# Kernel tuning notes

Hardware: AMD Instinct MI355X
Metric: run time of the kernel (lower is better)

The kernel has to match this reference:

```python
import jax, jax.numpy as jnp
import numpy as np

H = 1024
N_HEADS = 8
HEAD_DIM = H // N_HEADS
META_DIM = 256
VOCAB = 32000
MIN_W, MAX_W = 0.1, 5.0
LN_EPS = 1e-5


def _ln(x, g, b):
    mu = jnp.mean(x, axis=-1, keepdims=True)
    var = jnp.var(x, axis=-1, keepdims=True)
    return (x - mu) * jax.lax.rsqrt(var + LN_EPS) * g + b


def setup_inputs() -> dict:
    key = jax.random.key(0)
    ks = jax.random.split(key, 16)
    B, S = 4, 2048
    s = 0.02
    return {
        "hidden_states": jax.random.normal(ks[0], (B, S, H), jnp.float32),
        "token_ids": jax.random.randint(ks[1], (B, S), 0, VOCAB, jnp.int32),
        "attention_mask": jnp.ones((B, S), jnp.bool_),
        "pos_embed": jax.random.normal(ks[2], (1, S, H), jnp.float32),
        # torch nn.MultiheadAttention params
        "in_proj_w": jax.random.normal(ks[3], (3 * H, H), jnp.float32) * s,
        "in_proj_b": jnp.zeros((3 * H,), jnp.float32),
        "out_w": jax.random.normal(ks[4], (H, H), jnp.float32) * s,
        "out_b": jnp.zeros((H,), jnp.float32),
        # meta_network params (torch Linear convention: y = x @ W.T + b)
        "w1": jax.random.normal(ks[5], (META_DIM, 2 * H), jnp.float32) * s,
        "b1": jnp.zeros((META_DIM,), jnp.float32),
        "g1": jnp.ones((META_DIM,), jnp.float32),
        "beta1": jnp.zeros((META_DIM,), jnp.float32),
        "w2": jax.random.normal(ks[6], (META_DIM // 2, META_DIM), jnp.float32) * s,
        "b2": jnp.zeros((META_DIM // 2,), jnp.float32),
        "g2": jnp.ones((META_DIM // 2,), jnp.float32),
        "beta2": jnp.zeros((META_DIM // 2,), jnp.float32),
        "w3": jax.random.normal(ks[7], (1, META_DIM // 2), jnp.float32) * s,
        "b3": jnp.zeros((1,), jnp.float32),
        # tensorized ImportanceMemory.get_importance: one scalar per vocab id
        "importance_table": jax.random.uniform(ks[8], (VOCAB,), jnp.float32) * 0.1,
    }


def reference(hidden_states, token_ids, attention_mask, pos_embed,
              in_proj_w, in_proj_b, out_w, out_b,
              w1, b1, g1, beta1, w2, b2, g2, beta2, w3, b3,
              importance_table):
    B, S, _ = hidden_states.shape
    x = hidden_states + pos_embed[:, :S, :]

    # MultiheadAttention (batch_first, eval mode -> no dropout)
    qkv = x @ in_proj_w.T + in_proj_b                      # [B,S,3H]
    q, k, v = jnp.split(qkv, 3, axis=-1)
    q = q.reshape(B, S, N_HEADS, HEAD_DIM)
    k = k.reshape(B, S, N_HEADS, HEAD_DIM)
    v = v.reshape(B, S, N_HEADS, HEAD_DIM)
    scores = jnp.einsum('bqhd,bkhd->bhqk', q, k) / jnp.sqrt(jnp.float32(HEAD_DIM))
    scores = jnp.where(attention_mask[:, None, None, :], scores, jnp.float32(-1e9))
    attn = jax.nn.softmax(scores, axis=-1)
    ctx = jnp.einsum('bhqk,bkhd->bqhd', attn, v).reshape(B, S, H)
    attended = ctx @ out_w.T + out_b

    combined = jnp.concatenate([x, attended], axis=-1)     # [B,S,2H]
    h = jax.nn.relu(_ln(combined @ w1.T + b1, g1, beta1))
    h = jax.nn.relu(_ln(h @ w2.T + b2, g2, beta2))
    base_weights = (h @ w3.T + b3).squeeze(-1)             # [B,S]

    # tensorized per-token importance lookup + clamp (manual_weights empty)
    importance = importance_table[token_ids]               # gather [B,S]
    weight = jnp.clip(base_weights * (1.0 + importance), MIN_W, MAX_W)
    return jnp.where(attention_mask, weight, 0.0)
```

## Files before the change

kernel.cpp:

```cpp
#include <hip/hip_runtime.h>
#include <hip/hip_bf16.h>
#include <math.h>

typedef __bf16 bf16;
typedef bf16 bf16x8 __attribute__((ext_vector_type(8)));
typedef bf16 bf16x4 __attribute__((ext_vector_type(4)));
typedef float f32x4 __attribute__((ext_vector_type(4)));

#define HDIM 1024
#define NHEADS 8
#define HD 128
#define MD1 256
#define MD2 128
#define LNEPS 1e-5f

__device__ __forceinline__ f32x4 mfma16(bf16x8 a, bf16x8 b, f32x4 c) {
  return __builtin_amdgcn_mfma_f32_16x16x32_bf16(a, b, c, 0, 0, 0);
}

__device__ __forceinline__ void gload_lds16(const bf16* g, bf16* l) {
  __builtin_amdgcn_global_load_lds(
      (const __attribute__((address_space(1))) void*)g,
      (__attribute__((address_space(3))) void*)l, 16, 0, 0);
}

__global__ void k_prep_all(
    const float* __restrict__ hs, const float* __restrict__ pos,
    bf16* __restrict__ xbf, int SH, int nprep,
    const float* __restrict__ s0, bf16* __restrict__ d0, int n0,
    const float* __restrict__ s1, bf16* __restrict__ d1, int n1,
    const float* __restrict__ s2, bf16* __restrict__ d2, int n2,
    const float* __restrict__ s3, bf16* __restrict__ d3, int n3) {
  int i = (blockIdx.x * blockDim.x + threadIdx.x) * 4;
  if (i < nprep) {
    float4 a = *(const float4*)(hs + i);
    float4 p = *(const float4*)(pos + (i % SH));
    bf16x4 o;
    o[0] = (bf16)(a.x + p.x); o[1] = (bf16)(a.y + p.y);
    o[2] = (bf16)(a.z + p.z); o[3] = (bf16)(a.w + p.w);
    *(bf16x4*)(xbf + i) = o;
    return;
  }
  int j = i - nprep;
  const float* s; bf16* d;
  if (j < n0)                { s = s0 + j; d = d0 + j; }
  else if (j < n0 + n1)      { s = s1 + (j - n0); d = d1 + (j - n0); }
  else if (j < n0 + n1 + n2) { s = s2 + (j - n0 - n1); d = d2 + (j - n0 - n1); }
  else                       { s = s3 + (j - n0 - n1 - n2); d = d3 + (j - n0 - n1 - n2); }
  float4 v = *(const float4*)s;
  bf16x4 o;
  o[0] = (bf16)v.x; o[1] = (bf16)v.y; o[2] = (bf16)v.z; o[3] = (bf16)v.w;
  *(bf16x4*)d = o;
}

template<bool OUT_BF>
__global__ __launch_bounds__(256) void k_gemm128(
    const bf16* __restrict__ A, const bf16* __restrict__ Bw,
    const float* __restrict__ bias, void* __restrict__ out,
    int N, int K) {
  __shared__ bf16 As[128 * 32];
  __shared__ bf16 Bs[128 * 32];
  const int tid = threadIdx.x;
  const int w = tid >> 6, lane = tid & 63;
  const int quad = lane >> 4, l16 = lane & 15;
  const int wm = w & 1, wn = w >> 1;
  const int tm = blockIdx.x * 128, tn = blockIdx.y * 128;

  const int r0 = tid >> 2;
  const int f0 = (r0 ^ (r0 >> 2)) & 3;
  const int f1 = ((r0 + 64) ^ ((r0 + 64) >> 2)) & 3;
  const int c0 = (((tid & 3) ^ f0) * 8);
  const int c1 = (((tid & 3) ^ f1) * 8);
  const bf16* a0 = A + (size_t)(tm + r0) * K + c0;
  const bf16* a1 = A + (size_t)(tm + r0 + 64) * K + c1;
  const bf16* b0 = Bw + (size_t)(tn + r0) * K + c0;
  const bf16* b1 = Bw + (size_t)(tn + r0 + 64) * K + c1;
  bf16* lA = As + (size_t)tid * 8;
  bf16* lB = Bs + (size_t)tid * 8;

  f32x4 acc[4][4] = {};
  for (int k0 = 0; k0 < K; k0 += 32) {
    gload_lds16(a0 + k0, lA);
    gload_lds16(a1 + k0, lA + 2048);
    gload_lds16(b0 + k0, lB);
    gload_lds16(b1 + k0, lB + 2048);
    __syncthreads();
    bf16x8 af[4], bfr[4];
#pragma unroll
    for (int mt = 0; mt < 4; ++mt) {
      const int r = wm * 64 + mt * 16 + l16;
      af[mt] = *(const bf16x8*)&As[r * 32 + ((quad ^ ((r ^ (r >> 2)) & 3)) << 3)];
    }
#pragma unroll
    for (int nt = 0; nt < 4; ++nt) {
      const int r = wn * 64 + nt * 16 + l16;
      bfr[nt] = *(const bf16x8*)&Bs[r * 32 + ((quad ^ ((r ^ (r >> 2)) & 3)) << 3)];
    }
#pragma unroll
    for (int mt = 0; mt < 4; ++mt)
#pragma unroll
      for (int nt = 0; nt < 4; ++nt)
        acc[mt][nt] = mfma16(af[mt], bfr[nt], acc[mt][nt]);
    __syncthreads();
  }

#pragma unroll
  for (int nt = 0; nt < 4; ++nt) {
    const int col = tn + wn * 64 + nt * 16 + l16;
    const float bv = bias ? bias[col] : 0.f;
#pragma unroll
    for (int mt = 0; mt < 4; ++mt) {
#pragma unroll
      for (int i = 0; i < 4; ++i) {
        const int row = tm + wm * 64 + mt * 16 + quad * 4 + i;
        const float v = acc[mt][nt][i] + bv;
        if (OUT_BF) ((bf16*)out)[(size_t)row * N + col] = (bf16)v;
        else        ((float*)out)[(size_t)row * N + col] = v;
      }
    }
  }
}

__global__ __launch_bounds__(256) void k_gemm_qkv(
    const bf16* __restrict__ A, const bf16* __restrict__ Bw,
    const float* __restrict__ bias, bf16* __restrict__ Qo,
    bf16* __restrict__ Ko, bf16* __restrict__ VTo, int S, int K) {
  __shared__ bf16 As[128 * 32];
  __shared__ bf16 Bs[128 * 32];
  const int tid = threadIdx.x;
  const int w = tid >> 6, lane = tid & 63;
  const int quad = lane >> 4, l16 = lane & 15;
  const int wm = w & 1, wn = w >> 1;
  const int tm = blockIdx.x * 128, tn = blockIdx.y * 128;

  const int r0 = tid >> 2;
  const int f0 = (r0 ^ (r0 >> 2)) & 3;
  const int f1 = ((r0 + 64) ^ ((r0 + 64) >> 2)) & 3;
  const int c0 = (((tid & 3) ^ f0) * 8);
  const int c1 = (((tid & 3) ^ f1) * 8);
  const bf16* a0 = A + (size_t)(tm + r0) * K + c0;
  const bf16* a1 = A + (size_t)(tm + r0 + 64) * K + c1;
  const bf16* b0 = Bw + (size_t)(tn + r0) * K + c0;
  const bf16* b1 = Bw + (size_t)(tn + r0 + 64) * K + c1;
  bf16* lA = As + (size_t)tid * 8;
  bf16* lB = Bs + (size_t)tid * 8;

  f32x4 acc[4][4] = {};
  for (int k0 = 0; k0 < K; k0 += 32) {
    gload_lds16(a0 + k0, lA);
    gload_lds16(a1 + k0, lA + 2048);
    gload_lds16(b0 + k0, lB);
    gload_lds16(b1 + k0, lB + 2048);
    __syncthreads();
    bf16x8 af[4], bfr[4];
#pragma unroll
    for (int mt = 0; mt < 4; ++mt) {
      const int r = wm * 64 + mt * 16 + l16;
      af[mt] = *(const bf16x8*)&As[r * 32 + ((quad ^ ((r ^ (r >> 2)) & 3)) << 3)];
    }
#pragma unroll
    for (int nt = 0; nt < 4; ++nt) {
      const int r = wn * 64 + nt * 16 + l16;
      bfr[nt] = *(const bf16x8*)&Bs[r * 32 + ((quad ^ ((r ^ (r >> 2)) & 3)) << 3)];
    }
#pragma unroll
    for (int mt = 0; mt < 4; ++mt)
#pragma unroll
      for (int nt = 0; nt < 4; ++nt)
        acc[mt][nt] = mfma16(af[mt], bfr[nt], acc[mt][nt]);
    __syncthreads();
  }

  const int region = tn >> 10;
  const int btile = tm / S, s0 = tm % S;
#pragma unroll
  for (int nt = 0; nt < 4; ++nt) {
    const int col = tn + wn * 64 + nt * 16 + l16;
    const float bv = bias[col];
#pragma unroll
    for (int mt = 0; mt < 4; ++mt) {
      if (region == 2) {
        const int d = col - 2048, hh = d >> 7, dd = d & 127;
        const int sb = s0 + wm * 64 + mt * 16 + quad * 4;
        bf16x4 o4;
#pragma unroll
        for (int i = 0; i < 4; ++i) o4[i] = (bf16)(acc[mt][nt][i] + bv);
        *(bf16x4*)&VTo[((size_t)(btile * NHEADS + hh) * HD + dd) * S + sb] = o4;
      } else {
        bf16* dst = (region == 0) ? Qo : Ko;
        const int cc = (region == 0) ? col : col - 1024;
#pragma unroll
        for (int i = 0; i < 4; ++i) {
          const int row = tm + wm * 64 + mt * 16 + quad * 4 + i;
          dst[(size_t)row * HDIM + cc] = (bf16)(acc[mt][nt][i] + bv);
        }
      }
    }
  }
}

__global__ __launch_bounds__(256) void k_flash(
    const bf16* __restrict__ Qg, const bf16* __restrict__ Kg,
    const bf16* __restrict__ VTg, const int* __restrict__ mask,
    bf16* __restrict__ opart, float* __restrict__ lpart, int S, int Mtot) {
  __shared__ bf16 Ks[64][136];
  __shared__ bf16 Vt[128 * 64];
  __shared__ bf16 Ps[8 * 1024];
  __shared__ float biass[64];
  const int tid = threadIdx.x, w = tid >> 6, lane = tid & 63;
  const int quad = lane >> 4, l16 = lane & 15;
  const int bh = blockIdx.y, b = bh / NHEADS, h = bh % NHEADS;
  const int split = blockIdx.z;
  const int klo = split * (S >> 1), khi = klo + (S >> 1);
  const int q0 = blockIdx.x * 128 + w * 32;
  const size_t bS = (size_t)b * S;
  const bf16* Qb = Qg + bS * HDIM + h * HD;
  const bf16* Kb = Kg + bS * HDIM + h * HD;
  const bf16* Vb = VTg + (size_t)bh * HD * S;
  const int* mrow = mask + bS;
  bf16* op = opart + (size_t)split * Mtot * HDIM;
  float* lp = lpart + (size_t)split * Mtot * NHEADS;

  bf16x8 qf[2][4];
#pragma unroll
  for (int qt = 0; qt < 2; ++qt)
#pragma unroll
    for (int s = 0; s < 4; ++s)
      qf[qt][s] = *(const bf16x8*)(Qb + (size_t)(q0 + qt * 16 + l16) * HDIM + s * 32 + quad * 8);

  float lsum[2][4] = {};
  f32x4 o[2][8] = {};
  const float scale2 = 0.08838834764831845f * 1.4426950408889634f;

  bf16x8 kreg[4], vreg[4];
  int mreg = (tid < 64) ? mrow[klo + tid] : 0;
#pragma unroll
  for (int it = 0; it < 4; ++it) {
    const int cid = tid + it * 256;
    kreg[it] = *(const bf16x8*)(Kb + (size_t)(klo + (cid >> 4)) * HDIM + (cid & 15) * 8);
    vreg[it] = *(const bf16x8*)(Vb + (size_t)(cid >> 3) * S + klo + (cid & 7) * 8);
  }

  for (int key0 = klo; key0 < khi; key0 += 64) {
    __syncthreads();
#pragma unroll
    for (int it = 0; it < 4; ++it) {
      const int cid = tid + it * 256;
      *(bf16x8*)&Ks[cid >> 4][(cid & 15) * 8] = kreg[it];
      const int vd = cid >> 3, vkb = cid & 7;
      *(bf16x8*)&Vt[vd * 64 + ((vkb ^ (vd & 7)) << 3)] = vreg[it];
    }
    if (tid < 64) biass[tid] = mreg ? 0.f : -1e9f;
    __syncthreads();
    const int key0n = (key0 + 64 < khi) ? key0 + 64 : key0;
    if (tid < 64) mreg = mrow[key0n + tid];
#pragma unroll
    for (int it = 0; it < 4; ++it) {
      const int cid = tid + it * 256;
      kreg[it] = *(const bf16x8*)(Kb + (size_t)(key0n + (cid >> 4)) * HDIM + (cid & 15) * 8);
      vreg[it] = *(const bf16x8*)(Vb + (size_t)(cid >> 3) * S + key0n + (cid & 7) * 8);
    }
    f32x4 s4[2][4] = {};
#pragma unroll
    for (int g = 0; g < 4; ++g)
#pragma unroll
      for (int s = 0; s < 4; ++s) {
        bf16x8 kf = *(const bf16x8*)&Ks[g * 16 + l16][s * 32 + quad * 8];
        s4[0][g] = mfma16(qf[0][s], kf, s4[0][g]);
        s4[1][g] = mfma16(qf[1][s], kf, s4[1][g]);
      }
#pragma unroll
    for (int qt = 0; qt < 2; ++qt) {
      const int base = (w * 2 + qt) * 1024;
#pragma unroll
      for (int g = 0; g < 4; ++g) {
        const float bias = biass[g * 16 + l16];
        const int kb2 = 2 * g + (l16 >> 3), klo2 = l16 & 7;
#pragma unroll
        for (int i = 0; i < 4; ++i) {
          const float p = exp2f(fmaf(s4[qt][g][i], scale2, bias));
          lsum[qt][i] += p;
          const int r = quad * 4 + i, fr = (r ^ (r >> 3)) & 7;
          Ps[base + r * 64 + ((kb2 ^ fr) << 3) + klo2] = (bf16)p;
        }
      }
    }
    const int fl = (l16 ^ (l16 >> 3)) & 7;
#pragma unroll
    for (int hh = 0; hh < 2; ++hh) {
      const int kb = hh * 4 + quad;
      bf16x8 pf0 = *(const bf16x8*)&Ps[(w * 2) * 1024 + l16 * 64 + ((kb ^ fl) << 3)];
      bf16x8 pf1 = *(const bf16x8*)&Ps[(w * 2 + 1) * 1024 + l16 * 64 + ((kb ^ fl) << 3)];
#pragma unroll
      for (int dg = 0; dg < 8; ++dg) {
        const int d = dg * 16 + l16;
        bf16x8 vf = *(const bf16x8*)&Vt[d * 64 + ((kb ^ (d & 7)) << 3)];
        o[0][dg] = mfma16(pf0, vf, o[0][dg]);
        o[1][dg] = mfma16(pf1, vf, o[1][dg]);
      }
    }
  }

#pragma unroll
  for (int qt = 0; qt < 2; ++qt)
#pragma unroll
    for (int i = 0; i < 4; ++i) {
      float ls = lsum[qt][i];
#pragma unroll
      for (int off = 1; off < 16; off <<= 1) ls += __shfl_xor(ls, off);
      const int row = q0 + qt * 16 + quad * 4 + i;
      if (l16 == 0) lp[(bS + row) * NHEADS + h] = ls;
#pragma unroll
      for (int dg = 0; dg < 8; ++dg)
        op[(bS + row) * HDIM + h * HD + dg * 16 + l16] = (bf16)o[qt][dg][i];
    }
}

__global__ void k_combine(bf16* __restrict__ op0, const bf16* __restrict__ op1,
                          const float* __restrict__ lpart, int Mtot) {
  const int idx = (blockIdx.x * blockDim.x + threadIdx.x) * 4;
  const int row = idx >> 10;
  const int h = (idx & 1023) >> 7;
  const float l = lpart[row * NHEADS + h] +
                  lpart[(size_t)Mtot * NHEADS + row * NHEADS + h];
  const float inv = 1.0f / l;
  bf16x4 a = *(const bf16x4*)&op0[idx];
  bf16x4 b = *(const bf16x4*)&op1[idx];
  bf16x4 o;
#pragma unroll
  for (int j = 0; j < 4; ++j) o[j] = (bf16)(((float)a[j] + (float)b[j]) * inv);
  *(bf16x4*)&op0[idx] = o;
}

__global__ __launch_bounds__(256) void k_meta12(
    const bf16* __restrict__ A1, const bf16* __restrict__ A2,
    const bf16* __restrict__ Bw1, const float* __restrict__ b1,
    const float* __restrict__ g1, const float* __restrict__ be1,
    const bf16* __restrict__ Bw2, const float* __restrict__ b2,
    const float* __restrict__ g2, const float* __restrict__ be2,
    const float* __restrict__ w3, const float* __restrict__ b3,
    const int* __restrict__ tok, const int* __restrict__ msk,
    const float* __restrict__ imp, float* __restrict__ out) {
  __shared__ char smem[44032];
  __shared__ float part_s[64][4];
  __shared__ float part_q[64][4];
  bf16 (*As)[40]  = (bf16(*)[40])smem;
  bf16 (*Bs)[40]  = (bf16(*)[40])(smem + 5120);
  bf16 (*h1s)[264] = (bf16(*)[264])smem;
  bf16 (*Bs2)[40] = (bf16(*)[40])(smem + 33792);
  const int tid = threadIdx.x;
  const int w = tid >> 6, lane = tid & 63;
  const int quad = lane >> 4, l16 = lane & 15;
  const int tm = blockIdx.x * 64;
  const int lr = tid >> 2, lc = (tid & 3) * 8;

  f32x4 acc[4][4] = {};
  for (int k0 = 0; k0 < 2048; k0 += 32) {
    const int kg = k0 + lc;
    const bf16* ap = (kg < 1024) ? (A1 + (size_t)(tm + lr) * 1024 + kg)
                                 : (A2 + (size_t)(tm + lr) * 1024 + (kg - 1024));
    *(bf16x8*)&As[lr][lc] = *(const bf16x8*)ap;
#pragma unroll
    for (int it = 0; it < 4; ++it)
      *(bf16x8*)&Bs[lr + it * 64][lc] =
          *(const bf16x8*)(Bw1 + (size_t)(lr + it * 64) * 2048 + kg);
    __syncthreads();
    bf16x8 af[4], bfr[4];
#pragma unroll
    for (int mt = 0; mt < 4; ++mt) af[mt] = *(const bf16x8*)&As[mt * 16 + l16][quad * 8];
#pragma unroll
    for (int nt = 0; nt < 4; ++nt)
      bfr[nt] = *(const bf16x8*)&Bs[w * 64 + nt * 16 + l16][quad * 8];
#pragma unroll
    for (int mt = 0; mt < 4; ++mt)
#pragma unroll
      for (int nt = 0; nt < 4; ++nt)
        acc[mt][nt] = mfma16(af[mt], bfr[nt], acc[mt][nt]);
    __syncthreads();
  }

  float bv[4], gv[4], bev[4];
#pragma unroll
  for (int nt = 0; nt < 4; ++nt) {
    const int col = w * 64 + nt * 16 + l16;
    bv[nt] = b1[col]; gv[nt] = g1[col]; bev[nt] = be1[col];
  }
#pragma unroll
  for (int mt = 0; mt < 4; ++mt)
#pragma unroll
    for (int i = 0; i < 4; ++i) {
      float s = 0.f, q = 0.f;
#pragma unroll
      for (int nt = 0; nt < 4; ++nt) {
        const float v = acc[mt][nt][i] + bv[nt];
        s += v; q += v * v;
      }
#pragma unroll
      for (int off = 1; off < 16; off <<= 1) { s += __shfl_xor(s, off); q += __shfl_xor(q, off); }
      if (l16 == 0) {
        const int row = mt * 16 + quad * 4 + i;
        part_s[row][w] = s; part_q[row][w] = q;
      }
    }
  __syncthreads();
#pragma unroll
  for (int mt = 0; mt < 4; ++mt)
#pragma unroll
    for (int i = 0; i < 4; ++i) {
      const int row = mt * 16 + quad * 4 + i;
      const float4 ps = *(const float4*)part_s[row];
      const float4 pq = *(const float4*)part_q[row];
      const float sum = ps.x + ps.y + ps.z + ps.w;
      const float sq = pq.x + pq.y + pq.z + pq.w;
      const float mean = sum / MD1;
      const float var = sq / MD1 - mean * mean;
      const float r = rsqrtf(var + LNEPS);
#pragma unroll
      for (int nt = 0; nt < 4; ++nt) {
        const int col = w * 64 + nt * 16 + l16;
        const float v = acc[mt][nt][i] + bv[nt];
        const float t = (v - mean) * r * gv[nt] + bev[nt];
        h1s[row][col] = (bf16)fmaxf(t, 0.f);
      }
    }
  __syncthreads();

  f32x4 acc2[8] = {};
  for (int k0 = 0; k0 < MD1; k0 += 32) {
    const int kg = k0 + lc;
#pragma unroll
    for (int it = 0; it < 2; ++it)
      *(bf16x8*)&Bs2[lr + it * 64][lc] =
          *(const bf16x8*)(Bw2 + (size_t)(lr + it * 64) * MD1 + kg);
    __syncthreads();
    bf16x8 af = *(const bf16x8*)&h1s[w * 16 + l16][k0 + quad * 8];
#pragma unroll
    for (int nt = 0; nt < 8; ++nt) {
      bf16x8 bfr = *(const bf16x8*)&Bs2[nt * 16 + l16][quad * 8];
      acc2[nt] = mfma16(af, bfr, acc2[nt]);
    }
    __syncthreads();
  }

  float bv2[8], gv2[8], bev2[8], w3v[8];
#pragma unroll
  for (int nt = 0; nt < 8; ++nt) {
    const int col = nt * 16 + l16;
    bv2[nt] = b2[col]; gv2[nt] = g2[col]; bev2[nt] = be2[col]; w3v[nt] = w3[col];
  }
  const float b3v = b3[0];
#pragma unroll
  for (int i = 0; i < 4; ++i) {
    float s = 0.f, q = 0.f;
#pragma unroll
    for (int nt = 0; nt < 8; ++nt) {
      const float v = acc2[nt][i] + bv2[nt];
      s += v; q += v * v;
    }
#pragma unroll
    for (int off = 1; off < 16; off <<= 1) { s += __shfl_xor(s, off); q += __shfl_xor(q, off); }
    const float mean = s / MD2;
    const float var = q / MD2 - mean * mean;
    const float r = rsqrtf(var + LNEPS);
    float d = 0.f;
#pragma unroll
    for (int nt = 0; nt < 8; ++nt) {
      const float v = acc2[nt][i] + bv2[nt];
      const float t = (v - mean) * r * gv2[nt] + bev2[nt];
      d += fmaxf(t, 0.f) * w3v[nt];
    }
#pragma unroll
    for (int off = 1; off < 16; off <<= 1) d += __shfl_xor(d, off);
    if (l16 == 0) {
      const int row = tm + w * 16 + quad * 4 + i;
      const float base = d + b3v;
      float wt = base * (1.f + imp[tok[row]]);
      wt = fminf(fmaxf(wt, 0.1f), 5.0f);
      out[row] = msk[row] ? wt : 0.f;
    }
  }
}

extern "C" void kernel_launch(void* const* d_in, const int* in_sizes, int n_in,
                              void* d_out, int out_size, void* d_ws, size_t ws_size,
                              hipStream_t stream) {
  const float* hs  = (const float*)d_in[0];
  const int*   tok = (const int*)d_in[1];
  const int*   msk = (const int*)d_in[2];
  const float* pos = (const float*)d_in[3];
  const float* inw = (const float*)d_in[4];
  const float* inb = (const float*)d_in[5];
  const float* ow  = (const float*)d_in[6];
  const float* ob  = (const float*)d_in[7];
  const float* w1  = (const float*)d_in[8];
  const float* b1  = (const float*)d_in[9];
  const float* g1  = (const float*)d_in[10];
  const float* be1 = (const float*)d_in[11];
  const float* w2  = (const float*)d_in[12];
  const float* b2  = (const float*)d_in[13];
  const float* g2  = (const float*)d_in[14];
  const float* be2 = (const float*)d_in[15];
  const float* w3  = (const float*)d_in[16];
  const float* b3  = (const float*)d_in[17];
  const float* imp = (const float*)d_in[18];

  const int SH = in_sizes[3];
  const int S  = SH / HDIM;
  const int Bsz = in_sizes[0] / SH;
  const int M = Bsz * S;

  char* ws = (char*)d_ws;
  const size_t MB2 = (size_t)M * HDIM * 2;
  size_t off = 0;
  bf16* xbf = (bf16*)(ws + off);  off += MB2;
  bf16* Qb  = (bf16*)(ws + off);  off += MB2;
  bf16* Kb  = (bf16*)(ws + off);  off += MB2;
  bf16* VTb = (bf16*)(ws + off);  off += MB2;
  bf16* op0 = (bf16*)(ws + off);  off += MB2;
  bf16* op1 = (bf16*)(ws + off);  off += MB2;
  bf16* winp = (bf16*)(ws + off); off += (size_t)3 * HDIM * HDIM * 2;
  bf16* wout = (bf16*)(ws + off); off += (size_t)HDIM * HDIM * 2;
  bf16* w1b = (bf16*)(ws + off);  off += (size_t)MD1 * 2 * HDIM * 2;
  bf16* w2b = (bf16*)(ws + off);  off += (size_t)MD2 * MD1 * 2;
  float* lpart = (float*)(ws + off); off += (size_t)2 * M * NHEADS * 4;
  bf16* attbf = Qb;

  const int nprep = M * HDIM;
  const int n0 = 3 * HDIM * HDIM, n1 = HDIM * HDIM, n2 = MD1 * 2 * HDIM, n3 = MD2 * MD1;
  k_prep_all<<<(nprep + n0 + n1 + n2 + n3) / 4 / 256, 256, 0, stream>>>(
      hs, pos, xbf, SH, nprep, inw, winp, n0, ow, wout, n1, w1, w1b, n2, w2, w2b, n3);
  k_gemm_qkv<<<dim3(M / 128, (3 * HDIM) / 128), 256, 0, stream>>>(
      xbf, winp, inb, Qb, Kb, VTb, S, HDIM);
  k_flash<<<dim3(S / 128, Bsz * NHEADS, 2), 256, 0, stream>>>(
      Qb, Kb, VTb, msk, op0, lpart, S, M);
  k_combine<<<(M * HDIM / 4) / 256, 256, 0, stream>>>(op0, op1, lpart, M);
  k_gemm128<true><<<dim3(M / 128, HDIM / 128), 256, 0, stream>>>(
      op0, wout, ob, attbf, HDIM, HDIM);
  k_meta12<<<M / 64, 256, 0, stream>>>(xbf, attbf, w1b, b1, g1, be1,
                                       w2b, b2, g2, be2, w3, b3, tok, msk, imp,
                                       (float*)d_out);
}
```

Before: 435.6 us.

## Fold out-projection into meta W1, drop flash KV split, widen QKV K-tile

The attention out-projection is folded algebraically into the first meta layer by precomputing W1[:,H:] @ out_w and an adjusted bias, which removes the full M×H×H out-projection GEMM and its intermediate buffer. Flash attention no longer splits keys into two halves, so the combine kernel goes away and normalization happens in the epilogue. P is now built transposed so it can be written with vector stores. The QKV GEMM uses a 64-wide K tile with an 8-way swizzle. In exchange, the grid for flash attention is halved, which may lower occupancy, and the precomputed W' product is rounded to bf16.

```diff
diff --git a/kernel.cpp b/kernel.cpp
--- a/kernel.cpp
+++ b/kernel.cpp
@@ -53,121 +53,113 @@
   *(bf16x4*)d = o;
 }
 
-template<bool OUT_BF>
-__global__ __launch_bounds__(256) void k_gemm128(
+__global__ void k_b1p(const float* __restrict__ w1, const float* __restrict__ ob,
+                      const float* __restrict__ b1, float* __restrict__ b1p) {
+  const int t = threadIdx.x;
+  const int n = blockIdx.x * 64 + (t >> 2);
+  const int jq = t & 3;
+  const float* row = w1 + (size_t)n * 2048 + 1024 + jq * 256;
+  const float* obp = ob + jq * 256;
+  float acc = 0.f;
+  for (int j = 0; j < 256; j += 4) {
+    float4 a = *(const float4*)(row + j);
+    float4 o = *(const float4*)(obp + j);
+    acc += a.x * o.x + a.y * o.y + a.z * o.z + a.w * o.w;
+  }
+  acc += __shfl_xor(acc, 1);
+  acc += __shfl_xor(acc, 2);
+  if (jq == 0) b1p[n] = b1[n] + acc;
+}
+
+__global__ __launch_bounds__(256) void k_wprime(
+    const bf16* __restrict__ w1full, const bf16* __restrict__ ow,
+    bf16* __restrict__ Wp) {
+  __shared__ bf16 Bst[64][40];
+  const int tid = threadIdx.x;
+  const int w = tid >> 6, lane = tid & 63;
+  const int quad = lane >> 4, l16 = lane & 15;
+  const int d0 = blockIdx.x * 64, n0 = blockIdx.y * 64;
+  const bf16* arow = w1full + (size_t)(n0 + w * 16 + l16) * 2048 + 1024;
+  f32x4 acc[4] = {};
+  for (int k0 = 0; k0 < 1024; k0 += 32) {
+    const int kk = tid >> 3, dd8 = (tid & 7) * 8;
+    bf16x8 v = *(const bf16x8*)(ow + (size_t)(k0 + kk) * 1024 + d0 + dd8);
+    __syncthreads();
+#pragma unroll
+    for (int jj = 0; jj < 8; ++jj) Bst[dd8 + jj][kk] = v[jj];
+    __syncthreads();
+    bf16x8 af = *(const bf16x8*)(arow + k0 + quad * 8);
+#pragma unroll
+    for (int dg = 0; dg < 4; ++dg) {
+      bf16x8 bfr = *(const bf16x8*)&Bst[dg * 16 + l16][quad * 8];
+      acc[dg] = mfma16(af, bfr, acc[dg]);
+    }
+  }
+#pragma unroll
+  for (int dg = 0; dg < 4; ++dg) {
+    const int d = d0 + dg * 16 + l16;
+#pragma unroll
+    for (int i = 0; i < 4; ++i)
+      Wp[(size_t)(n0 + w * 16 + quad * 4 + i) * 1024 + d] = (bf16)acc[dg][i];
+  }
+}
+
+__global__ __launch_bounds__(256) void k_gemm_qkv(
     const bf16* __restrict__ A, const bf16* __restrict__ Bw,
-    const float* __restrict__ bias, void* __restrict__ out,
-    int N, int K) {
-  __shared__ bf16 As[128 * 32];
-  __shared__ bf16 Bs[128 * 32];
+    const float* __restrict__ bias, bf16* __restrict__ Qo,
+    bf16* __restrict__ Ko, bf16* __restrict__ VTo, int S, int K) {
+  __shared__ bf16 As[128 * 64];
+  __shared__ bf16 Bs[128 * 64];
   const int tid = threadIdx.x;
   const int w = tid >> 6, lane = tid & 63;
   const int quad = lane >> 4, l16 = lane & 15;
   const int wm = w & 1, wn = w >> 1;
   const int tm = blockIdx.x * 128, tn = blockIdx.y * 128;
 
-  const int r0 = tid >> 2;
-  const int f0 = (r0 ^ (r0 >> 2)) & 3;
-  const int f1 = ((r0 + 64) ^ ((r0 + 64) >> 2)) & 3;
-  const int c0 = (((tid & 3) ^ f0) * 8);
-  const int c1 = (((tid & 3) ^ f1) * 8);
-  const bf16* a0 = A + (size_t)(tm + r0) * K + c0;
-  const bf16* a1 = A + (size_t)(tm + r0 + 64) * K + c1;
-  const bf16* b0 = Bw + (size_t)(tn + r0) * K + c0;
-  const bf16* b1 = Bw + (size_t)(tn + r0 + 64) * K + c1;
+  const int tq = tid >> 3, t8 = tid & 7;
+  const bf16 *ap[4], *bp[4];
+#pragma unroll
+  for (int c = 0; c < 4; ++c) {
+    const int r = c * 32 + tq;
+    const int col = ((t8 ^ ((r ^ (r >> 3)) & 7)) * 8);
+    ap[c] = A + (size_t)(tm + r) * K + col;
+    bp[c] = Bw + (size_t)(tn + r) * K + col;
+  }
   bf16* lA = As + (size_t)tid * 8;
   bf16* lB = Bs + (size_t)tid * 8;
 
+  int fam[4], fbn[4], ram[4], rbn[4];
+#pragma unroll
+  for (int mt = 0; mt < 4; ++mt) {
+    const int r = wm * 64 + mt * 16 + l16;
+    ram[mt] = r; fam[mt] = (r ^ (r >> 3)) & 7;
+    const int r2 = wn * 64 + mt * 16 + l16;
+    rbn[mt] = r2; fbn[mt] = (r2 ^ (r2 >> 3)) & 7;
+  }
+
   f32x4 acc[4][4] = {};
-  for (int k0 = 0; k0 < K; k0 += 32) {
-    gload_lds16(a0 + k0, lA);
-    gload_lds16(a1 + k0, lA + 2048);
-    gload_lds16(b0 + k0, lB);
-    gload_lds16(b1 + k0, lB + 2048);
-    __syncthreads();
-    bf16x8 af[4], bfr[4];
-#pragma unroll
-    for (int mt = 0; mt < 4; ++mt) {
-      const int r = wm * 64 + mt * 16 + l16;
-      af[mt] = *(const bf16x8*)&As[r * 32 + ((quad ^ ((r ^ (r >> 2)) & 3)) << 3)];
-    }
-#pragma unroll
-    for (int nt = 0; nt < 4; ++nt) {
-      const int r = wn * 64 + nt * 16 + l16;
-      bfr[nt] = *(const bf16x8*)&Bs[r * 32 + ((quad ^ ((r ^ (r >> 2)) & 3)) << 3)];
-    }
-#pragma unroll
-    for (int mt = 0; mt < 4; ++mt)
+  for (int k0 = 0; k0 < K; k0 += 64) {
+#pragma unroll
+    for (int c = 0; c < 4; ++c) {
+      gload_lds16(ap[c] + k0, lA + c * 2048);
+      gload_lds16(bp[c] + k0, lB + c * 2048);
+    }
+    __syncthreads();
+#pragma unroll
+    for (int ks = 0; ks < 2; ++ks) {
+      bf16x8 af[4], bfr[4];
+#pragma unroll
+      for (int mt = 0; mt < 4; ++mt)
+        af[mt] = *(const bf16x8*)&As[ram[mt] * 64 + (((ks * 4 + quad) ^ fam[mt]) << 3)];
 #pragma unroll
       for (int nt = 0; nt < 4; ++nt)
-        acc[mt][nt] = mfma16(af[mt], bfr[nt], acc[mt][nt]);
-    __syncthreads();
-  }
-
-#pragma unroll
-  for (int nt = 0; nt < 4; ++nt) {
-    const int col = tn + wn * 64 + nt * 16 + l16;
-    const float bv = bias ? bias[col] : 0.f;
-#pragma unroll
-    for (int mt = 0; mt < 4; ++mt) {
-#pragma unroll
-      for (int i = 0; i < 4; ++i) {
-        const int row = tm + wm * 64 + mt * 16 + quad * 4 + i;
-        const float v = acc[mt][nt][i] + bv;
-        if (OUT_BF) ((bf16*)out)[(size_t)row * N + col] = (bf16)v;
-        else        ((float*)out)[(size_t)row * N + col] = v;
-      }
-    }
-  }
-}
-
-__global__ __launch_bounds__(256) void k_gemm_qkv(
-    const bf16* __restrict__ A, const bf16* __restrict__ Bw,
-    const float* __restrict__ bias, bf16* __restrict__ Qo,
-    bf16* __restrict__ Ko, bf16* __restrict__ VTo, int S, int K) {
-  __shared__ bf16 As[128 * 32];
-  __shared__ bf16 Bs[128 * 32];
-  const int tid = threadIdx.x;
-  const int w = tid >> 6, lane = tid & 63;
-  const int quad = lane >> 4, l16 = lane & 15;
-  const int wm = w & 1, wn = w >> 1;
-  const int tm = blockIdx.x * 128, tn = blockIdx.y * 128;
-
-  const int r0 = tid >> 2;
-  const int f0 = (r0 ^ (r0 >> 2)) & 3;
-  const int f1 = ((r0 + 64) ^ ((r0 + 64) >> 2)) & 3;
-  const int c0 = (((tid & 3) ^ f0) * 8);
-  const int c1 = (((tid & 3) ^ f1) * 8);
-  const bf16* a0 = A + (size_t)(tm + r0) * K + c0;
-  const bf16* a1 = A + (size_t)(tm + r0 + 64) * K + c1;
-  const bf16* b0 = Bw + (size_t)(tn + r0) * K + c0;
-  const bf16* b1 = Bw + (size_t)(tn + r0 + 64) * K + c1;
-  bf16* lA = As + (size_t)tid * 8;
-  bf16* lB = Bs + (size_t)tid * 8;
-
-  f32x4 acc[4][4] = {};
-  for (int k0 = 0; k0 < K; k0 += 32) {
-    gload_lds16(a0 + k0, lA);
-    gload_lds16(a1 + k0, lA + 2048);
-    gload_lds16(b0 + k0, lB);
-    gload_lds16(b1 + k0, lB + 2048);
-    __syncthreads();
-    bf16x8 af[4], bfr[4];
-#pragma unroll
-    for (int mt = 0; mt < 4; ++mt) {
-      const int r = wm * 64 + mt * 16 + l16;
-      af[mt] = *(const bf16x8*)&As[r * 32 + ((quad ^ ((r ^ (r >> 2)) & 3)) << 3)];
-    }
-#pragma unroll
-    for (int nt = 0; nt < 4; ++nt) {
-      const int r = wn * 64 + nt * 16 + l16;
-      bfr[nt] = *(const bf16x8*)&Bs[r * 32 + ((quad ^ ((r ^ (r >> 2)) & 3)) << 3)];
-    }
-#pragma unroll
-    for (int mt = 0; mt < 4; ++mt)
-#pragma unroll
-      for (int nt = 0; nt < 4; ++nt)
-        acc[mt][nt] = mfma16(af[mt], bfr[nt], acc[mt][nt]);
+        bfr[nt] = *(const bf16x8*)&Bs[rbn[nt] * 64 + (((ks * 4 + quad) ^ fbn[nt]) << 3)];
+#pragma unroll
+      for (int mt = 0; mt < 4; ++mt)
+#pragma unroll
+        for (int nt = 0; nt < 4; ++nt)
+          acc[mt][nt] = mfma16(af[mt], bfr[nt], acc[mt][nt]);
+    }
     __syncthreads();
   }
 
@@ -202,7 +194,7 @@
 __global__ __launch_bounds__(256) void k_flash(
     const bf16* __restrict__ Qg, const bf16* __restrict__ Kg,
     const bf16* __restrict__ VTg, const int* __restrict__ mask,
-    bf16* __restrict__ opart, float* __restrict__ lpart, int S, int Mtot) {
+    bf16* __restrict__ ctx, int S) {
   __shared__ bf16 Ks[64][136];
   __shared__ bf16 Vt[128 * 64];
   __shared__ bf16 Ps[8 * 1024];
@@ -210,16 +202,12 @@
   const int tid = threadIdx.x, w = tid >> 6, lane = tid & 63;
   const int quad = lane >> 4, l16 = lane & 15;
   const int bh = blockIdx.y, b = bh / NHEADS, h = bh % NHEADS;
-  const int split = blockIdx.z;
-  const int klo = split * (S >> 1), khi = klo + (S >> 1);
   const int q0 = blockIdx.x * 128 + w * 32;
   const size_t bS = (size_t)b * S;
   const bf16* Qb = Qg + bS * HDIM + h * HD;
   const bf16* Kb = Kg + bS * HDIM + h * HD;
   const bf16* Vb = VTg + (size_t)bh * HD * S;
   const int* mrow = mask + bS;
-  bf16* op = opart + (size_t)split * Mtot * HDIM;
-  float* lp = lpart + (size_t)split * Mtot * NHEADS;
 
   bf16x8 qf[2][4];
 #pragma unroll
@@ -228,20 +216,21 @@
     for (int s = 0; s < 4; ++s)
       qf[qt][s] = *(const bf16x8*)(Qb + (size_t)(q0 + qt * 16 + l16) * HDIM + s * 32 + quad * 8);
 
-  float lsum[2][4] = {};
+  float lsum[2] = {0.f, 0.f};
   f32x4 o[2][8] = {};
   const float scale2 = 0.08838834764831845f * 1.4426950408889634f;
 
+  const int nchunk = S / 64;
   bf16x8 kreg[4], vreg[4];
-  int mreg = (tid < 64) ? mrow[klo + tid] : 0;
+  int mreg = (tid < 64) ? mrow[tid] : 0;
 #pragma unroll
   for (int it = 0; it < 4; ++it) {
     const int cid = tid + it * 256;
-    kreg[it] = *(const bf16x8*)(Kb + (size_t)(klo + (cid >> 4)) * HDIM + (cid & 15) * 8);
-    vreg[it] = *(const bf16x8*)(Vb + (size_t)(cid >> 3) * S + klo + (cid & 7) * 8);
-  }
-
-  for (int key0 = klo; key0 < khi; key0 += 64) {
+    kreg[it] = *(const bf16x8*)(Kb + (size_t)(cid >> 4) * HDIM + (cid & 15) * 8);
+    vreg[it] = *(const bf16x8*)(Vb + (size_t)(cid >> 3) * S + (cid & 7) * 8);
+  }
+
+  for (int c0 = 0; c0 < nchunk; ++c0) {
     __syncthreads();
 #pragma unroll
     for (int it = 0; it < 4; ++it) {
@@ -252,7 +241,7 @@
     }
     if (tid < 64) biass[tid] = mreg ? 0.f : -1e9f;
     __syncthreads();
-    const int key0n = (key0 + 64 < khi) ? key0 + 64 : key0;
+    const int key0n = ((c0 + 1 < nchunk) ? c0 + 1 : c0) * 64;
     if (tid < 64) mreg = mrow[key0n + tid];
 #pragma unroll
     for (int it = 0; it < 4; ++it) {
@@ -266,31 +255,30 @@
 #pragma unroll
       for (int s = 0; s < 4; ++s) {
         bf16x8 kf = *(const bf16x8*)&Ks[g * 16 + l16][s * 32 + quad * 8];
-        s4[0][g] = mfma16(qf[0][s], kf, s4[0][g]);
-        s4[1][g] = mfma16(qf[1][s], kf, s4[1][g]);
+        s4[0][g] = mfma16(kf, qf[0][s], s4[0][g]);
+        s4[1][g] = mfma16(kf, qf[1][s], s4[1][g]);
       }
 #pragma unroll
     for (int qt = 0; qt < 2; ++qt) {
       const int base = (w * 2 + qt) * 1024;
 #pragma unroll
       for (int g = 0; g < 4; ++g) {
-        const float bias = biass[g * 16 + l16];
-        const int kb2 = 2 * g + (l16 >> 3), klo2 = l16 & 7;
+        bf16x4 pk;
 #pragma unroll
         for (int i = 0; i < 4; ++i) {
-          const float p = exp2f(fmaf(s4[qt][g][i], scale2, bias));
-          lsum[qt][i] += p;
-          const int r = quad * 4 + i, fr = (r ^ (r >> 3)) & 7;
-          Ps[base + r * 64 + ((kb2 ^ fr) << 3) + klo2] = (bf16)p;
+          const float p = exp2f(fmaf(s4[qt][g][i], scale2, biass[g * 16 + quad * 4 + i]));
+          lsum[qt] += p;
+          pk[i] = (bf16)p;
         }
-      }
-    }
-    const int fl = (l16 ^ (l16 >> 3)) & 7;
-#pragma unroll
-    for (int hh = 0; hh < 2; ++hh) {
-      const int kb = hh * 4 + quad;
-      bf16x8 pf0 = *(const bf16x8*)&Ps[(w * 2) * 1024 + l16 * 64 + ((kb ^ fl) << 3)];
-      bf16x8 pf1 = *(const bf16x8*)&Ps[(w * 2 + 1) * 1024 + l16 * 64 + ((kb ^ fl) << 3)];
+        const int sw = (2 * g + (quad >> 1)) ^ (l16 & 7);
+        *(bf16x4*)&Ps[base + l16 * 64 + sw * 8 + (quad & 1) * 4] = pk;
+      }
+    }
+#pragma unroll
+    for (int kk = 0; kk < 2; ++kk) {
+      const int kb = kk * 4 + quad;
+      bf16x8 pf0 = *(const bf16x8*)&Ps[(w * 2) * 1024 + l16 * 64 + ((kb ^ (l16 & 7)) << 3)];
+      bf16x8 pf1 = *(const bf16x8*)&Ps[(w * 2 + 1) * 1024 + l16 * 64 + ((kb ^ (l16 & 7)) << 3)];
 #pragma unroll
       for (int dg = 0; dg < 8; ++dg) {
         const int d = dg * 16 + l16;
@@ -302,40 +290,28 @@
   }
 
 #pragma unroll
+  for (int qt = 0; qt < 2; ++qt) {
+    lsum[qt] += __shfl_xor(lsum[qt], 16);
+    lsum[qt] += __shfl_xor(lsum[qt], 32);
+  }
+#pragma unroll
   for (int qt = 0; qt < 2; ++qt)
 #pragma unroll
     for (int i = 0; i < 4; ++i) {
-      float ls = lsum[qt][i];
-#pragma unroll
-      for (int off = 1; off < 16; off <<= 1) ls += __shfl_xor(ls, off);
+      const float ls = __shfl(lsum[qt], quad * 4 + i);
+      const float inv = 1.0f / ls;
       const int row = q0 + qt * 16 + quad * 4 + i;
-      if (l16 == 0) lp[(bS + row) * NHEADS + h] = ls;
 #pragma unroll
       for (int dg = 0; dg < 8; ++dg)
-        op[(bS + row) * HDIM + h * HD + dg * 16 + l16] = (bf16)o[qt][dg][i];
-    }
-}
-
-__global__ void k_combine(bf16* __restrict__ op0, const bf16* __restrict__ op1,
-                          const float* __restrict__ lpart, int Mtot) {
-  const int idx = (blockIdx.x * blockDim.x + threadIdx.x) * 4;
-  const int row = idx >> 10;
-  const int h = (idx & 1023) >> 7;
-  const float l = lpart[row * NHEADS + h] +
-                  lpart[(size_t)Mtot * NHEADS + row * NHEADS + h];
-  const float inv = 1.0f / l;
-  bf16x4 a = *(const bf16x4*)&op0[idx];
-  bf16x4 b = *(const bf16x4*)&op1[idx];
-  bf16x4 o;
-#pragma unroll
-  for (int j = 0; j < 4; ++j) o[j] = (bf16)(((float)a[j] + (float)b[j]) * inv);
-  *(bf16x4*)&op0[idx] = o;
+        ctx[(bS + row) * HDIM + h * HD + dg * 16 + l16] = (bf16)(o[qt][dg][i] * inv);
+    }
 }
 
 __global__ __launch_bounds__(256) void k_meta12(
     const bf16* __restrict__ A1, const bf16* __restrict__ A2,
-    const bf16* __restrict__ Bw1, const float* __restrict__ b1,
-    const float* __restrict__ g1, const float* __restrict__ be1,
+    const bf16* __restrict__ Bw1, const bf16* __restrict__ Wp,
+    const float* __restrict__ b1p, const float* __restrict__ g1,
+    const float* __restrict__ be1,
     const bf16* __restrict__ Bw2, const float* __restrict__ b2,
     const float* __restrict__ g2, const float* __restrict__ be2,
     const float* __restrict__ w3, const float* __restrict__ b3,
@@ -361,9 +337,12 @@
                                  : (A2 + (size_t)(tm + lr) * 1024 + (kg - 1024));
     *(bf16x8*)&As[lr][lc] = *(const bf16x8*)ap;
 #pragma unroll
-    for (int it = 0; it < 4; ++it)
-      *(bf16x8*)&Bs[lr + it * 64][lc] =
-          *(const bf16x8*)(Bw1 + (size_t)(lr + it * 64) * 2048 + kg);
+    for (int it = 0; it < 4; ++it) {
+      const int row = lr + it * 64;
+      const bf16* bp = (kg < 1024) ? (Bw1 + (size_t)row * 2048 + kg)
+                                   : (Wp + (size_t)row * 1024 + (kg - 1024));
+      *(bf16x8*)&Bs[row][lc] = *(const bf16x8*)bp;
+    }
     __syncthreads();
     bf16x8 af[4], bfr[4];
 #pragma unroll
@@ -383,7 +362,7 @@
 #pragma unroll
   for (int nt = 0; nt < 4; ++nt) {
     const int col = w * 64 + nt * 16 + l16;
-    bv[nt] = b1[col]; gv[nt] = g1[col]; bev[nt] = be1[col];
+    bv[nt] = b1p[col]; gv[nt] = g1[col]; bev[nt] = be1[col];
   }
 #pragma unroll
   for (int mt = 0; mt < 4; ++mt)
@@ -473,8 +452,7 @@
     for (int off = 1; off < 16; off <<= 1) d += __shfl_xor(d, off);
     if (l16 == 0) {
       const int row = tm + w * 16 + quad * 4 + i;
-      const float base = d + b3v;
-      float wt = base * (1.f + imp[tok[row]]);
+      float wt = (d + b3v) * (1.f + imp[tok[row]]);
       wt = fminf(fmaxf(wt, 0.1f), 5.0f);
       out[row] = msk[row] ? wt : 0.f;
     }
@@ -516,27 +494,24 @@
   bf16* Qb  = (bf16*)(ws + off);  off += MB2;
   bf16* Kb  = (bf16*)(ws + off);  off += MB2;
   bf16* VTb = (bf16*)(ws + off);  off += MB2;
-  bf16* op0 = (bf16*)(ws + off);  off += MB2;
-  bf16* op1 = (bf16*)(ws + off);  off += MB2;
+  bf16* ctx = (bf16*)(ws + off);  off += MB2;
   bf16* winp = (bf16*)(ws + off); off += (size_t)3 * HDIM * HDIM * 2;
   bf16* wout = (bf16*)(ws + off); off += (size_t)HDIM * HDIM * 2;
   bf16* w1b = (bf16*)(ws + off);  off += (size_t)MD1 * 2 * HDIM * 2;
   bf16* w2b = (bf16*)(ws + off);  off += (size_t)MD2 * MD1 * 2;
-  float* lpart = (float*)(ws + off); off += (size_t)2 * M * NHEADS * 4;
-  bf16* attbf = Qb;
+  bf16* Wp  = (bf16*)(ws + off);  off += (size_t)MD1 * HDIM * 2;
+  float* b1p = (float*)(ws + off); off += (size_t)MD1 * 4;
 
   const int nprep = M * HDIM;
   const int n0 = 3 * HDIM * HDIM, n1 = HDIM * HDIM, n2 = MD1 * 2 * HDIM, n3 = MD2 * MD1;
   k_prep_all<<<(nprep + n0 + n1 + n2 + n3) / 4 / 256, 256, 0, stream>>>(
       hs, pos, xbf, SH, nprep, inw, winp, n0, ow, wout, n1, w1, w1b, n2, w2, w2b, n3);
+  k_b1p<<<MD1 / 64, 256, 0, stream>>>(w1, ob, b1, b1p);
+  k_wprime<<<dim3(HDIM / 64, MD1 / 64), 256, 0, stream>>>(w1b, wout, Wp);
   k_gemm_qkv<<<dim3(M / 128, (3 * HDIM) / 128), 256, 0, stream>>>(
       xbf, winp, inb, Qb, Kb, VTb, S, HDIM);
-  k_flash<<<dim3(S / 128, Bsz * NHEADS, 2), 256, 0, stream>>>(
-      Qb, Kb, VTb, msk, op0, lpart, S, M);
-  k_combine<<<(M * HDIM / 4) / 256, 256, 0, stream>>>(op0, op1, lpart, M);
-  k_gemm128<true><<<dim3(M / 128, HDIM / 128), 256, 0, stream>>>(
-      op0, wout, ob, attbf, HDIM, HDIM);
-  k_meta12<<<M / 64, 256, 0, stream>>>(xbf, attbf, w1b, b1, g1, be1,
+  k_flash<<<dim3(S / 128, Bsz * NHEADS), 256, 0, stream>>>(Qb, Kb, VTb, msk, ctx, S);
+  k_meta12<<<M / 64, 256, 0, stream>>>(xbf, ctx, w1b, Wp, b1p, g1, be1,
                                        w2b, b2, g2, be2, w3, b3, tok, msk, imp,
                                        (float*)d_out);
 }
```

Result: faster. 382.7 us (-12.1%).
